# Kernel optimization log

Hardware: AMD Instinct MI355X
Metric: run time of the kernel (lower is better)

Reference implementation:

```python
import jax, jax.numpy as jnp
import numpy as np

N_NODES = 50000
N_RAND_EDGES = 1_600_000
IN_F = 512
HID = 64
HEADS = 8
N_CLASSES = 20
SLOPE = 0.2  # LeakyReLU negative slope


def setup_inputs() -> dict:
    key = jax.random.key(0)
    ks = jax.random.split(key, 6)
    x = jax.random.normal(ks[0], (N_NODES, IN_F), dtype=jnp.float32)
    er = jax.random.randint(ks[1], (2, N_RAND_EDGES), 0, N_NODES)
    loops = jnp.tile(jnp.arange(N_NODES), (2, 1))  # self-loops so every row of adj is nonzero
    edge_index = jnp.concatenate([er, loops], axis=1)  # [2, E]
    # Learned parameters (per SpGraphAttentionLayer: weight [in,out], alpha [1,2*out] -> stored flat)
    W1 = jax.random.normal(ks[2], (HEADS, IN_F, HID), dtype=jnp.float32) * 0.05
    a1 = jax.random.normal(ks[3], (HEADS, 2 * HID), dtype=jnp.float32) * 0.1
    W2 = jax.random.normal(ks[4], (HEADS * HID, N_CLASSES), dtype=jnp.float32) * 0.05
    a2 = jax.random.normal(ks[5], (2 * N_CLASSES,), dtype=jnp.float32) * 0.1
    return {"x": x, "W1": W1, "a1": a1, "W2": W2, "a2": a2, "edge_index": edge_index}


def _gat_layer(x, W, a, e0, e1, n):
    # h = x @ weight; edge score = alpha . [h[src], h[dst]] computed as two per-node dots
    h = x @ W  # [N, F_out]
    f = W.shape[1]
    s_src = h @ a[:f]   # [N]
    s_dst = h @ a[f:]   # [N]
    edge_e = jnp.exp(jax.nn.leaky_relu(s_src[e0] + s_dst[e1], SLOPE))  # [E]
    rowsum = jax.ops.segment_sum(edge_e, e0, num_segments=n)  # spmm(adj_e, ones)
    agg = jax.ops.segment_sum(edge_e[:, None] * h[e1], e0, num_segments=n)  # spmm(adj_e, h)
    return agg / rowsum[:, None]


def reference(x, W1, a1, W2, a2, edge_index):
    n = x.shape[0]
    e0, e1 = edge_index[0], edge_index[1]
    # layer 1: per-head GAT, elu, concat along features (dropout is identity in eval)
    heads = [jax.nn.elu(_gat_layer(x, W1[i], a1[i], e0, e1, n)) for i in range(W1.shape[0])]
    hcat = jnp.concatenate(heads, axis=1)  # [N, HEADS*HID]
    out = jax.nn.elu(_gat_layer(hcat, W2, a2, e0, e1, n))  # [N, C]
    return out
```

## Files before the change

### kernel.cpp

```cpp
#include <hip/hip_runtime.h>
#include <hip/hip_fp16.h>
#include <math.h>

#define SLOPE 0.2f
#define SSHIFT 11

typedef short bf16x8 __attribute__((ext_vector_type(8)));
typedef float f32x4  __attribute__((ext_vector_type(4)));

static __device__ __forceinline__ float elu_f(float x){ return x > 0.f ? x : (__expf(x) - 1.f); }
static __device__ __forceinline__ float lrelu(float t){ return t > 0.f ? t : SLOPE*t; }
static __device__ __forceinline__ unsigned short f2bf_rne(float f){
    unsigned int u = __float_as_uint(f);
    unsigned int r = (u + 0x7FFFu + ((u >> 16) & 1u)) >> 16;
    return (unsigned short)r;
}
static __device__ __forceinline__ float bf2f(unsigned short h){ return __uint_as_float(((unsigned int)h) << 16); }

#define ASYNC_COPY16(gp, lp) \
    __builtin_amdgcn_global_load_lds((const __attribute__((address_space(1))) void*)(gp), \
                                     (__attribute__((address_space(3))) void*)(lp), 16, 0, 0)

__global__ void __launch_bounds__(256) hist_sliced_kernel(const int* __restrict__ e0, const int* __restrict__ e1,
                                                          int E, int n, int NS, int* __restrict__ cnt){
    const int s = blockIdx.x & 7;
    const int c = blockIdx.x >> 3;
    const int K = gridDim.x >> 3;
    const int lo = (int)((long)s*n >> 3), hi = (int)((long)(s+1)*n >> 3);
    const int i0 = (int)((long)c*E/K), i1 = (int)((long)(c+1)*E/K);
    for (int i = i0 + threadIdx.x; i < i1; i += 256){
        int j = e0[i];
        if (j >= lo && j < hi) atomicAdd(&cnt[j*NS + (e1[i] >> SSHIFT)], 1);
    }
}

__global__ void __launch_bounds__(256) scan_reduce_kernel(const int* __restrict__ cnt, int T, int* __restrict__ bsum){
    int c0 = blockIdx.x*4096 + threadIdx.x*16;
    int sum = 0;
    #pragma unroll
    for (int q = 0; q < 16; ++q){ int i = c0 + q; if (i < T) sum += cnt[i]; }
    #pragma unroll
    for (int off = 1; off < 64; off <<= 1) sum += __shfl_xor(sum, off, 64);
    __shared__ int ws_[4];
    int lane = threadIdx.x & 63, wid = threadIdx.x >> 6;
    if (lane == 0) ws_[wid] = sum;
    __syncthreads();
    if (threadIdx.x == 0) bsum[blockIdx.x] = ws_[0] + ws_[1] + ws_[2] + ws_[3];
}

__global__ void __launch_bounds__(512) scan_small_kernel(const int* __restrict__ bsum, int NB, int* __restrict__ bexcl){
    int t = threadIdx.x;
    int v = (t < NB) ? bsum[t] : 0;
    int lane = t & 63, wid = t >> 6;
    int val = v;
    #pragma unroll
    for (int off = 1; off < 64; off <<= 1){ int u = __shfl_up(val, off, 64); if (lane >= off) val += u; }
    __shared__ int wt[8];
    if (lane == 63) wt[wid] = val;
    __syncthreads();
    int base = 0;
    for (int w2 = 0; w2 < wid; ++w2) base += wt[w2];
    if (t < NB) bexcl[t] = base + val - v;
}

__global__ void __launch_bounds__(256) scan_apply_kernel(int* __restrict__ cnt_cur, int T,
                                                         const int* __restrict__ bexcl){
    int c0 = blockIdx.x*4096 + threadIdx.x*16;
    int v[16];
    #pragma unroll
    for (int q = 0; q < 16; ++q){ int i = c0 + q; v[q] = (i < T) ? cnt_cur[i] : 0; }
    int tsum = 0;
    #pragma unroll
    for (int q = 0; q < 16; ++q){ int t_ = v[q]; v[q] = tsum; tsum += t_; }
    int lane = threadIdx.x & 63, wid = threadIdx.x >> 6;
    int val = tsum;
    #pragma unroll
    for (int off = 1; off < 64; off <<= 1){ int u = __shfl_up(val, off, 64); if (lane >= off) val += u; }
    __shared__ int wt[4];
    if (lane == 63) wt[wid] = val;
    __syncthreads();
    int base = bexcl[blockIdx.x];
    for (int w2 = 0; w2 < wid; ++w2) base += wt[w2];
    base += val - tsum;
    #pragma unroll
    for (int q = 0; q < 16; ++q){ int i = c0 + q; if (i < T) cnt_cur[i] = base + v[q]; }
}

__global__ void __launch_bounds__(256) scatter_sliced_kernel(const int* __restrict__ e0, const int* __restrict__ e1,
                                                             int E, int n, int NS,
                                                             int* __restrict__ cursor, int* __restrict__ sidx){
    const int s = blockIdx.x & 7;
    const int c = blockIdx.x >> 3;
    const int K = gridDim.x >> 3;
    const int lo = (int)((long)s*n >> 3), hi = (int)((long)(s+1)*n >> 3);
    const int i0 = (int)((long)c*E/K), i1 = (int)((long)(c+1)*E/K);
    for (int i = i0 + threadIdx.x; i < i1; i += 256){
        int j = e0[i];
        if (j >= lo && j < hi){
            int jj = e1[i];
            int p = atomicAdd(&cursor[j*NS + (jj >> SSHIFT)], 1);
            sidx[p] = jj;
        }
    }
}

__global__ void __launch_bounds__(256) split_x_kernel(const float* __restrict__ x,
                                                      unsigned short* __restrict__ xhi,
                                                      unsigned short* __restrict__ xlo, int total4){
    int i = blockIdx.x*256 + threadIdx.x;
    if (i >= total4) return;
    float4 v = ((const float4*)x)[i];
    ushort4 h, l;
    h.x = f2bf_rne(v.x); l.x = f2bf_rne(v.x - bf2f(h.x));
    h.y = f2bf_rne(v.y); l.y = f2bf_rne(v.y - bf2f(h.y));
    h.z = f2bf_rne(v.z); l.z = f2bf_rne(v.z - bf2f(h.z));
    h.w = f2bf_rne(v.w); l.w = f2bf_rne(v.w - bf2f(h.w));
    ((ushort4*)xhi)[i] = h;
    ((ushort4*)xlo)[i] = l;
}

__global__ void __launch_bounds__(256) prep_w_kernel(const float* __restrict__ W1,
                                                     unsigned short* __restrict__ wThi,
                                                     unsigned short* __restrict__ wTlo){
    int idx = blockIdx.x*256 + threadIdx.x;
    int head = idx >> 15, rem = idx & 32767;
    int c = rem >> 9, k = rem & 511;
    float f = W1[((size_t)head << 15) + k*64 + c];
    unsigned short h = f2bf_rne(f);
    wThi[idx] = h;
    wTlo[idx] = f2bf_rne(f - bf2f(h));
}

__global__ void __launch_bounds__(256) gemm1_mfma_kernel(const unsigned short* __restrict__ xhi,
                                                         const unsigned short* __restrict__ xlo,
                                                         const unsigned short* __restrict__ wThi,
                                                         const unsigned short* __restrict__ wTlo,
                                                         const float* __restrict__ a1,
                                                         __half* __restrict__ h_g,
                                                         float* __restrict__ ssrc, float* __restrict__ sdst,
                                                         int n, int nwg){
    __shared__ unsigned short lds[16384];
    const int bid = blockIdx.x;
    const int xcd = bid & 7, jj = bid >> 3;
    const int q = nwg >> 3, r = nwg & 7;
    const int logical = (xcd < r ? xcd*(q+1) : r*(q+1) + (xcd-r)*q) + jj;
    const int rowtile = logical >> 2, ct = logical & 3;
    const int row0 = rowtile*128, col0 = ct*128;
    const int w = threadIdx.x >> 6, lane = threadIdx.x & 63;
    const int wm = w >> 1, wn = w & 1;
    const int lr = lane & 15, lk = lane >> 4;
    f32x4 acc[4][4] = {};
    const unsigned short* sbase[8];
    unsigned int soff[8];
    #pragma unroll
    for (int i = 0; i < 8; ++i){
        unsigned int off = w*8192u + i*1024u + lane*16u;
        unsigned int arr = off >> 13, within = off & 8191u;
        unsigned int rrow = within >> 6, kel = (within & 63u) >> 1;
        const unsigned short* g;
        size_t gidx;
        if (arr == 0)      { g = xhi;  gidx = (size_t)(row0 + rrow)*512 + kel; }
        else if (arr == 1) { g = xlo;  gidx = (size_t)(row0 + rrow)*512 + kel; }
        else if (arr == 2) { g = wThi; gidx = (size_t)(col0 + rrow)*512 + kel; }
        else               { g = wTlo; gidx = (size_t)(col0 + rrow)*512 + kel; }
        sbase[i] = g + gidx;
        soff[i] = (w*8192u + i*1024u);
    }
    const unsigned short* Ahi = lds;
    const unsigned short* Alo = lds + 4096;
    const unsigned short* Bhi = lds + 8192;
    const unsigned short* Blo = lds + 12288;
    for (int k0 = 0; k0 < 512; k0 += 32){
        #pragma unroll
        for (int i = 0; i < 8; ++i)
            ASYNC_COPY16(sbase[i] + k0, (char*)lds + soff[i]);
        __syncthreads();
        bf16x8 a_h[4], a_l[4], b_h[4], b_l[4];
        #pragma unroll
        for (int mi = 0; mi < 4; ++mi){
            int rowl = wm*64 + mi*16 + lr;
            a_h[mi] = *(const bf16x8*)(Ahi + rowl*32 + lk*8);
            a_l[mi] = *(const bf16x8*)(Alo + rowl*32 + lk*8);
        }
        #pragma unroll
        for (int ni = 0; ni < 4; ++ni){
            int coll = wn*64 + ni*16 + lr;
            b_h[ni] = *(const bf16x8*)(Bhi + coll*32 + lk*8);
            b_l[ni] = *(const bf16x8*)(Blo + coll*32 + lk*8);
        }
        #pragma unroll
        for (int mi = 0; mi < 4; ++mi)
            #pragma unroll
            for (int ni = 0; ni < 4; ++ni){
                f32x4& A = acc[mi][ni];
                A = __builtin_amdgcn_mfma_f32_16x16x32_bf16(a_h[mi], b_h[ni], A, 0, 0, 0);
                A = __builtin_amdgcn_mfma_f32_16x16x32_bf16(a_h[mi], b_l[ni], A, 0, 0, 0);
                A = __builtin_amdgcn_mfma_f32_16x16x32_bf16(a_l[mi], b_h[ni], A, 0, 0, 0);
            }
        __syncthreads();
    }
    const int head = ct*2 + wn;
    float as_[4], ad_[4];
    #pragma unroll
    for (int ni = 0; ni < 4; ++ni){
        as_[ni] = a1[(size_t)head*128 + ni*16 + lr];
        ad_[ni] = a1[(size_t)head*128 + 64 + ni*16 + lr];
    }
    #pragma unroll
    for (int mi = 0; mi < 4; ++mi){
        #pragma unroll
        for (int reg = 0; reg < 4; ++reg){
            float s = 0.f, d = 0.f;
            #pragma unroll
            for (int ni = 0; ni < 4; ++ni){
                float v = acc[mi][ni][reg];
                s += v*as_[ni]; d += v*ad_[ni];
            }
            s += __shfl_xor(s, 1); d += __shfl_xor(d, 1);
            s += __shfl_xor(s, 2); d += __shfl_xor(d, 2);
            s += __shfl_xor(s, 4); d += __shfl_xor(d, 4);
            s += __shfl_xor(s, 8); d += __shfl_xor(d, 8);
            const int node = row0 + wm*64 + mi*16 + lk*4 + reg;
            if (node < n){
                #pragma unroll
                for (int ni = 0; ni < 4; ++ni)
                    h_g[(size_t)node*512 + head*64 + ni*16 + lr] = __float2half(acc[mi][ni][reg]);
                if (lr == 0){
                    ssrc[(size_t)node*8 + head] = s;
                    sdst[(size_t)node*8 + head] = d;
                }
            }
        }
    }
}

__global__ void __launch_bounds__(256) agg1_kernel(const __half* __restrict__ h_g, const float* __restrict__ ssrc,
                                                   const float* __restrict__ sdst,
                                                   const int* __restrict__ bend, const int* __restrict__ sidx,
                                                   __half* __restrict__ hcat, int n, int NS){
    const int w = threadIdx.x >> 6, lane = threadIdx.x & 63;
    const int node = blockIdx.x*4 + w;
    if (node >= n) return;
    const int r0 = node ? bend[(size_t)node*NS - 1] : 0;
    const int r1 = bend[(size_t)(node+1)*NS - 1];
    const int h = lane >> 3;
    const float ssh = ssrc[(size_t)node*8 + h];
    float acc[8] = {};
    float wsum = 0.f;
    int e = r0;
    for (; e + 3 < r1; e += 4){
        int j0 = sidx[e], j1 = sidx[e+1], j2 = sidx[e+2], j3 = sidx[e+3];
        uint4 g0 = *(const uint4*)(h_g + (size_t)j0*512 + lane*8);
        uint4 g1 = *(const uint4*)(h_g + (size_t)j1*512 + lane*8);
        uint4 g2 = *(const uint4*)(h_g + (size_t)j2*512 + lane*8);
        uint4 g3 = *(const uint4*)(h_g + (size_t)j3*512 + lane*8);
        float s0 = sdst[(size_t)j0*8 + h], s1 = sdst[(size_t)j1*8 + h];
        float s2 = sdst[(size_t)j2*8 + h], s3 = sdst[(size_t)j3*8 + h];
        float w0 = __expf(lrelu(ssh + s0));
        float w1 = __expf(lrelu(ssh + s1));
        float w2 = __expf(lrelu(ssh + s2));
        float w3 = __expf(lrelu(ssh + s3));
        const unsigned int* u0 = &g0.x; const unsigned int* u1 = &g1.x;
        const unsigned int* u2 = &g2.x; const unsigned int* u3 = &g3.x;
        #pragma unroll
        for (int qq = 0; qq < 4; ++qq){
            float2 f0 = __half22float2(*(const __half2*)&u0[qq]);
            float2 f1 = __half22float2(*(const __half2*)&u1[qq]);
            float2 f2 = __half22float2(*(const __half2*)&u2[qq]);
            float2 f3 = __half22float2(*(const __half2*)&u3[qq]);
            acc[2*qq]   += w0*f0.x + w1*f1.x + w2*f2.x + w3*f3.x;
            acc[2*qq+1] += w0*f0.y + w1*f1.y + w2*f2.y + w3*f3.y;
        }
        wsum += (w0 + w1) + (w2 + w3);
    }
    for (; e < r1; ++e){
        int j = sidx[e];
        uint4 g = *(const uint4*)(h_g + (size_t)j*512 + lane*8);
        float wg = __expf(lrelu(ssh + sdst[(size_t)j*8 + h]));
        const unsigned int* u = &g.x;
        #pragma unroll
        for (int qq = 0; qq < 4; ++qq){
            float2 f = __half22float2(*(const __half2*)&u[qq]);
            acc[2*qq]   += wg*f.x;
            acc[2*qq+1] += wg*f.y;
        }
        wsum += wg;
    }
    float inv = 1.f / wsum;
    union { uint4 u; __half hv[8]; } pk;
    #pragma unroll
    for (int qq = 0; qq < 8; ++qq) pk.hv[qq] = __float2half(elu_f(acc[qq]*inv));
    *(uint4*)(hcat + (size_t)node*512 + lane*8) = pk.u;
}

__global__ void __launch_bounds__(256) gemm2_kernel(const __half* __restrict__ hcat, const float* __restrict__ W2,
                                                    const float* __restrict__ a2,
                                                    float* __restrict__ h2, float* __restrict__ ssrc,
                                                    float* __restrict__ sdst, int n){
    __shared__ float As[16][257];
    __shared__ float Ws[16][20];
    const int tid = threadIdx.x;
    const int node = blockIdx.x*256 + tid;
    float acc[20] = {};
    for (int k0 = 0; k0 < 512; k0 += 16){
        uint4 u0 = {0,0,0,0}, u1 = {0,0,0,0};
        if (node < n){
            const __half* src = hcat + (size_t)node*512 + k0;
            u0 = *(const uint4*)src;
            u1 = *(const uint4*)(src + 8);
        }
        const unsigned int* ua = &u0.x;
        const unsigned int* ub = &u1.x;
        #pragma unroll
        for (int qq = 0; qq < 4; ++qq){
            float2 f = __half22float2(*(const __half2*)&ua[qq]);
            As[2*qq][tid] = f.x; As[2*qq+1][tid] = f.y;
            float2 g = __half22float2(*(const __half2*)&ub[qq]);
            As[8+2*qq][tid] = g.x; As[8+2*qq+1][tid] = g.y;
        }
        for (int qq = tid; qq < 320; qq += 256){
            int kr = qq/20, cc = qq%20;
            Ws[kr][cc] = W2[(size_t)(k0 + kr)*20 + cc];
        }
        __syncthreads();
        #pragma unroll
        for (int kk = 0; kk < 16; ++kk){
            float a = As[kk][tid];
            #pragma unroll
            for (int cc = 0; cc < 20; ++cc) acc[cc] += a*Ws[kk][cc];
        }
        __syncthreads();
    }
    if (node < n){
        float s0 = 0.f, s1 = 0.f;
        #pragma unroll
        for (int cc = 0; cc < 20; ++cc){
            h2[(size_t)node*20 + cc] = acc[cc];
            s0 += acc[cc]*a2[cc];
            s1 += acc[cc]*a2[20 + cc];
        }
        ssrc[node] = s0; sdst[node] = s1;
    }
}

__global__ void __launch_bounds__(256) agg2_kernel(const float* __restrict__ h2, const float* __restrict__ ssrc,
                                                   const float* __restrict__ sdstv,
                                                   const int* __restrict__ bend, const int* __restrict__ sidx,
                                                   float* __restrict__ out, int n, int NS){
    const int w = threadIdx.x >> 6, lane = threadIdx.x & 63;
    const int node = blockIdx.x*4 + w;
    if (node >= n) return;
    const int r0 = node ? bend[(size_t)node*NS - 1] : 0;
    const int r1 = bend[(size_t)(node+1)*NS - 1];
    const float ss = ssrc[node];
    const bool act = lane < 20;
    float acc = 0.f, wsum = 0.f;
    int e = r0;
    for (; e + 3 < r1; e += 4){
        int j0 = sidx[e], j1 = sidx[e+1], j2 = sidx[e+2], j3 = sidx[e+3];
        float v0 = act ? h2[(size_t)j0*20 + lane] : 0.f;
        float v1 = act ? h2[(size_t)j1*20 + lane] : 0.f;
        float v2 = act ? h2[(size_t)j2*20 + lane] : 0.f;
        float v3 = act ? h2[(size_t)j3*20 + lane] : 0.f;
        float s0 = sdstv[j0], s1 = sdstv[j1], s2 = sdstv[j2], s3 = sdstv[j3];
        float w0 = __expf(lrelu(ss + s0));
        float w1 = __expf(lrelu(ss + s1));
        float w2 = __expf(lrelu(ss + s2));
        float w3 = __expf(lrelu(ss + s3));
        acc += w0*v0 + w1*v1 + w2*v2 + w3*v3;
        wsum += (w0 + w1) + (w2 + w3);
    }
    for (; e < r1; ++e){
        int j = sidx[e];
        float v = act ? h2[(size_t)j*20 + lane] : 0.f;
        float wg = __expf(lrelu(ss + sdstv[j]));
        acc += wg*v; wsum += wg;
    }
    if (act) out[(size_t)node*20 + lane] = elu_f(acc / wsum);
}

extern "C" void kernel_launch(void* const* d_in, const int* in_sizes, int n_in,
                              void* d_out, int out_size, void* d_ws, size_t ws_size,
                              hipStream_t stream){
    const float* x  = (const float*)d_in[0];
    const float* W1 = (const float*)d_in[1];
    const float* a1 = (const float*)d_in[2];
    const float* W2 = (const float*)d_in[3];
    const float* a2 = (const float*)d_in[4];
    const int*   ei = (const int*)d_in[5];
    const int n = in_sizes[0] / 512;
    const int E = in_sizes[5] / 2;
    const int* e0 = ei;
    const int* e1 = ei + E;
    const int NS = (n + (1 << SSHIFT) - 1) >> SSHIFT;
    const int T  = n * NS;

    char* p = (char*)d_ws;
    auto alloc = [&](size_t bytes)->char*{ char* r = p; p += (bytes + 255) & ~(size_t)255; return r; };
    unsigned short* xhi  = (unsigned short*)alloc((size_t)n*512*2);
    unsigned short* xlo  = (unsigned short*)alloc((size_t)n*512*2);
    __half*         h_g  = (__half*)        alloc((size_t)n*512*2);
    unsigned short* wThi = (unsigned short*)alloc((size_t)8*64*512*2);
    unsigned short* wTlo = (unsigned short*)alloc((size_t)8*64*512*2);
    float* ssrc1   = (float*)alloc((size_t)n*8*4);
    float* sdst1   = (float*)alloc((size_t)n*8*4);
    __half* hcat  = (__half*)xhi;
    float*  h2    = (float*)xlo;
    float*  ssrc2 = h2 + (size_t)n*20;
    float*  sdst2 = ssrc2 + n;
    int*    cursor = (int*)((char*)xlo + ((size_t)6 << 20));
    int*    sidx   = cursor + T;
    int*    bsum   = sidx + E;
    int*    bexcl  = bsum + 2048;

    const int total4 = n*512/4;
    split_x_kernel<<<(total4 + 255)/256, 256, 0, stream>>>(x, xhi, xlo, total4);
    prep_w_kernel <<<1024, 256, 0, stream>>>(W1, wThi, wTlo);
    const int mb = (n + 127)/128;
    const int nwg = mb*4;
    gemm1_mfma_kernel<<<nwg, 256, 0, stream>>>(xhi, xlo, wThi, wTlo, a1, h_g, ssrc1, sdst1, n, nwg);

    hipMemsetAsync(cursor, 0, (size_t)T*4, stream);
    const int KCH = 192;
    hist_sliced_kernel<<<KCH*8, 256, 0, stream>>>(e0, e1, E, n, NS, cursor);
    const int NB = (T + 4095)/4096;
    scan_reduce_kernel<<<NB, 256, 0, stream>>>(cursor, T, bsum);
    scan_small_kernel <<<1, 512, 0, stream>>>(bsum, NB, bexcl);
    scan_apply_kernel <<<NB, 256, 0, stream>>>(cursor, T, bexcl);
    scatter_sliced_kernel<<<KCH*8, 256, 0, stream>>>(e0, e1, E, n, NS, cursor, sidx);

    agg1_kernel<<<(n + 3)/4, 256, 0, stream>>>(h_g, ssrc1, sdst1, cursor, sidx, hcat, n, NS);
    const int nb256 = (n + 255)/256;
    gemm2_kernel<<<nb256, 256, 0, stream>>>(hcat, W2, a2, h2, ssrc2, sdst2, n);
    agg2_kernel <<<(n + 3)/4, 256, 0, stream>>>(h2, ssrc2, sdst2, cursor, sidx, (float*)d_out, n, NS);
}
```

Baseline: 835.3 us.

## Precompute per-edge attention weights in scatter, drop column sub-buckets in CSR build

The CSR build no longer sub-buckets each row by destination column slice. Histogram, scan and scatter now work on one counter per node, which shrinks the scan and memset. The scatter kernel now also computes the 8 per-head exp(leakyrelu) edge weights and stores them as bf16 in a per-edge array, so agg1 reads them instead of gathering sdst and computing exp per edge. Both aggregation kernels unroll to 8 edges. In exchange, the per-edge weights lose precision, the weight array adds E*16 bytes of write and read traffic, and the column-sorted locality inside each row that the sub-buckets gave is gone.

```diff
diff --git a/kernel.cpp b/kernel.cpp
--- a/kernel.cpp
+++ b/kernel.cpp
@@ -3,7 +3,6 @@
 #include <math.h>
 
 #define SLOPE 0.2f
-#define SSHIFT 11
 
 typedef short bf16x8 __attribute__((ext_vector_type(8)));
 typedef float f32x4  __attribute__((ext_vector_type(4)));
@@ -21,8 +20,8 @@
     __builtin_amdgcn_global_load_lds((const __attribute__((address_space(1))) void*)(gp), \
                                      (__attribute__((address_space(3))) void*)(lp), 16, 0, 0)
 
-__global__ void __launch_bounds__(256) hist_sliced_kernel(const int* __restrict__ e0, const int* __restrict__ e1,
-                                                          int E, int n, int NS, int* __restrict__ cnt){
+__global__ void __launch_bounds__(256) hist_sliced_kernel(const int* __restrict__ e0, int E, int n,
+                                                          int* __restrict__ cnt){
     const int s = blockIdx.x & 7;
     const int c = blockIdx.x >> 3;
     const int K = gridDim.x >> 3;
@@ -30,7 +29,7 @@
     const int i0 = (int)((long)c*E/K), i1 = (int)((long)(c+1)*E/K);
     for (int i = i0 + threadIdx.x; i < i1; i += 256){
         int j = e0[i];
-        if (j >= lo && j < hi) atomicAdd(&cnt[j*NS + (e1[i] >> SSHIFT)], 1);
+        if (j >= lo && j < hi) atomicAdd(&cnt[j], 1);
     }
 }
 
@@ -86,9 +85,11 @@
     for (int q = 0; q < 16; ++q){ int i = c0 + q; if (i < T) cnt_cur[i] = base + v[q]; }
 }
 
-__global__ void __launch_bounds__(256) scatter_sliced_kernel(const int* __restrict__ e0, const int* __restrict__ e1,
-                                                             int E, int n, int NS,
-                                                             int* __restrict__ cursor, int* __restrict__ sidx){
+__global__ void __launch_bounds__(256) scatter_w_kernel(const int* __restrict__ e0, const int* __restrict__ e1,
+                                                        int E, int n,
+                                                        const float* __restrict__ ssrc1, const float* __restrict__ sdst1,
+                                                        int* __restrict__ cursor, int* __restrict__ sidx,
+                                                        uint4* __restrict__ wgt8){
     const int s = blockIdx.x & 7;
     const int c = blockIdx.x >> 3;
     const int K = gridDim.x >> 3;
@@ -98,8 +99,27 @@
         int j = e0[i];
         if (j >= lo && j < hi){
             int jj = e1[i];
-            int p = atomicAdd(&cursor[j*NS + (jj >> SSHIFT)], 1);
+            int p = atomicAdd(&cursor[j], 1);
             sidx[p] = jj;
+            float4 sa0 = *(const float4*)(ssrc1 + (size_t)j*8);
+            float4 sa1 = *(const float4*)(ssrc1 + (size_t)j*8 + 4);
+            float4 sb0 = *(const float4*)(sdst1 + (size_t)jj*8);
+            float4 sb1 = *(const float4*)(sdst1 + (size_t)jj*8 + 4);
+            float w_[8];
+            w_[0] = __expf(lrelu(sa0.x + sb0.x));
+            w_[1] = __expf(lrelu(sa0.y + sb0.y));
+            w_[2] = __expf(lrelu(sa0.z + sb0.z));
+            w_[3] = __expf(lrelu(sa0.w + sb0.w));
+            w_[4] = __expf(lrelu(sa1.x + sb1.x));
+            w_[5] = __expf(lrelu(sa1.y + sb1.y));
+            w_[6] = __expf(lrelu(sa1.z + sb1.z));
+            w_[7] = __expf(lrelu(sa1.w + sb1.w));
+            uint4 pk;
+            pk.x = (unsigned)f2bf_rne(w_[0]) | ((unsigned)f2bf_rne(w_[1]) << 16);
+            pk.y = (unsigned)f2bf_rne(w_[2]) | ((unsigned)f2bf_rne(w_[3]) << 16);
+            pk.z = (unsigned)f2bf_rne(w_[4]) | ((unsigned)f2bf_rne(w_[5]) << 16);
+            pk.w = (unsigned)f2bf_rne(w_[6]) | ((unsigned)f2bf_rne(w_[7]) << 16);
+            wgt8[p] = pk;
         }
     }
 }
@@ -234,57 +254,54 @@
     }
 }
 
-__global__ void __launch_bounds__(256) agg1_kernel(const __half* __restrict__ h_g, const float* __restrict__ ssrc,
-                                                   const float* __restrict__ sdst,
+__global__ void __launch_bounds__(256) agg1_kernel(const __half* __restrict__ h_g,
+                                                   const unsigned short* __restrict__ wgt,
                                                    const int* __restrict__ bend, const int* __restrict__ sidx,
-                                                   __half* __restrict__ hcat, int n, int NS){
+                                                   __half* __restrict__ hcat, int n){
     const int w = threadIdx.x >> 6, lane = threadIdx.x & 63;
     const int node = blockIdx.x*4 + w;
     if (node >= n) return;
-    const int r0 = node ? bend[(size_t)node*NS - 1] : 0;
-    const int r1 = bend[(size_t)(node+1)*NS - 1];
+    const int r0 = node ? bend[node-1] : 0;
+    const int r1 = bend[node];
     const int h = lane >> 3;
-    const float ssh = ssrc[(size_t)node*8 + h];
     float acc[8] = {};
     float wsum = 0.f;
     int e = r0;
-    for (; e + 3 < r1; e += 4){
-        int j0 = sidx[e], j1 = sidx[e+1], j2 = sidx[e+2], j3 = sidx[e+3];
-        uint4 g0 = *(const uint4*)(h_g + (size_t)j0*512 + lane*8);
-        uint4 g1 = *(const uint4*)(h_g + (size_t)j1*512 + lane*8);
-        uint4 g2 = *(const uint4*)(h_g + (size_t)j2*512 + lane*8);
-        uint4 g3 = *(const uint4*)(h_g + (size_t)j3*512 + lane*8);
-        float s0 = sdst[(size_t)j0*8 + h], s1 = sdst[(size_t)j1*8 + h];
-        float s2 = sdst[(size_t)j2*8 + h], s3 = sdst[(size_t)j3*8 + h];
-        float w0 = __expf(lrelu(ssh + s0));
-        float w1 = __expf(lrelu(ssh + s1));
-        float w2 = __expf(lrelu(ssh + s2));
-        float w3 = __expf(lrelu(ssh + s3));
-        const unsigned int* u0 = &g0.x; const unsigned int* u1 = &g1.x;
-        const unsigned int* u2 = &g2.x; const unsigned int* u3 = &g3.x;
-        #pragma unroll
-        for (int qq = 0; qq < 4; ++qq){
-            float2 f0 = __half22float2(*(const __half2*)&u0[qq]);
-            float2 f1 = __half22float2(*(const __half2*)&u1[qq]);
-            float2 f2 = __half22float2(*(const __half2*)&u2[qq]);
-            float2 f3 = __half22float2(*(const __half2*)&u3[qq]);
-            acc[2*qq]   += w0*f0.x + w1*f1.x + w2*f2.x + w3*f3.x;
-            acc[2*qq+1] += w0*f0.y + w1*f1.y + w2*f2.y + w3*f3.y;
-        }
-        wsum += (w0 + w1) + (w2 + w3);
+    for (; e + 7 < r1; e += 8){
+        int j[8];
+        #pragma unroll
+        for (int qq = 0; qq < 8; ++qq) j[qq] = sidx[e+qq];
+        uint4 g[8];
+        #pragma unroll
+        for (int qq = 0; qq < 8; ++qq) g[qq] = *(const uint4*)(h_g + (size_t)j[qq]*512 + lane*8);
+        float wv[8];
+        #pragma unroll
+        for (int qq = 0; qq < 8; ++qq) wv[qq] = bf2f(wgt[(size_t)(e+qq)*8 + h]);
+        #pragma unroll
+        for (int qq = 0; qq < 8; ++qq){
+            const unsigned int* u = &g[qq].x;
+            float wq = wv[qq];
+            #pragma unroll
+            for (int p2 = 0; p2 < 4; ++p2){
+                float2 f = __half22float2(*(const __half2*)&u[p2]);
+                acc[2*p2]   += wq*f.x;
+                acc[2*p2+1] += wq*f.y;
+            }
+            wsum += wq;
+        }
     }
     for (; e < r1; ++e){
         int j = sidx[e];
         uint4 g = *(const uint4*)(h_g + (size_t)j*512 + lane*8);
-        float wg = __expf(lrelu(ssh + sdst[(size_t)j*8 + h]));
+        float wq = bf2f(wgt[(size_t)e*8 + h]);
         const unsigned int* u = &g.x;
         #pragma unroll
-        for (int qq = 0; qq < 4; ++qq){
-            float2 f = __half22float2(*(const __half2*)&u[qq]);
-            acc[2*qq]   += wg*f.x;
-            acc[2*qq+1] += wg*f.y;
-        }
-        wsum += wg;
+        for (int p2 = 0; p2 < 4; ++p2){
+            float2 f = __half22float2(*(const __half2*)&u[p2]);
+            acc[2*p2]   += wq*f.x;
+            acc[2*p2+1] += wq*f.y;
+        }
+        wsum += wq;
     }
     float inv = 1.f / wsum;
     union { uint4 u; __half hv[8]; } pk;
@@ -346,35 +363,37 @@
 __global__ void __launch_bounds__(256) agg2_kernel(const float* __restrict__ h2, const float* __restrict__ ssrc,
                                                    const float* __restrict__ sdstv,
                                                    const int* __restrict__ bend, const int* __restrict__ sidx,
-                                                   float* __restrict__ out, int n, int NS){
+                                                   float* __restrict__ out, int n){
     const int w = threadIdx.x >> 6, lane = threadIdx.x & 63;
     const int node = blockIdx.x*4 + w;
     if (node >= n) return;
-    const int r0 = node ? bend[(size_t)node*NS - 1] : 0;
-    const int r1 = bend[(size_t)(node+1)*NS - 1];
+    const int r0 = node ? bend[node-1] : 0;
+    const int r1 = bend[node];
     const float ss = ssrc[node];
     const bool act = lane < 20;
     float acc = 0.f, wsum = 0.f;
     int e = r0;
-    for (; e + 3 < r1; e += 4){
-        int j0 = sidx[e], j1 = sidx[e+1], j2 = sidx[e+2], j3 = sidx[e+3];
-        float v0 = act ? h2[(size_t)j0*20 + lane] : 0.f;
-        float v1 = act ? h2[(size_t)j1*20 + lane] : 0.f;
-        float v2 = act ? h2[(size_t)j2*20 + lane] : 0.f;
-        float v3 = act ? h2[(size_t)j3*20 + lane] : 0.f;
-        float s0 = sdstv[j0], s1 = sdstv[j1], s2 = sdstv[j2], s3 = sdstv[j3];
-        float w0 = __expf(lrelu(ss + s0));
-        float w1 = __expf(lrelu(ss + s1));
-        float w2 = __expf(lrelu(ss + s2));
-        float w3 = __expf(lrelu(ss + s3));
-        acc += w0*v0 + w1*v1 + w2*v2 + w3*v3;
-        wsum += (w0 + w1) + (w2 + w3);
+    for (; e + 7 < r1; e += 8){
+        int j[8];
+        #pragma unroll
+        for (int qq = 0; qq < 8; ++qq) j[qq] = sidx[e+qq];
+        float v[8], s[8];
+        #pragma unroll
+        for (int qq = 0; qq < 8; ++qq) v[qq] = act ? h2[(size_t)j[qq]*20 + lane] : 0.f;
+        #pragma unroll
+        for (int qq = 0; qq < 8; ++qq) s[qq] = sdstv[j[qq]];
+        #pragma unroll
+        for (int qq = 0; qq < 8; ++qq){
+            float wq = __expf(lrelu(ss + s[qq]));
+            acc += wq*v[qq];
+            wsum += wq;
+        }
     }
     for (; e < r1; ++e){
         int j = sidx[e];
         float v = act ? h2[(size_t)j*20 + lane] : 0.f;
-        float wg = __expf(lrelu(ss + sdstv[j]));
-        acc += wg*v; wsum += wg;
+        float wq = __expf(lrelu(ss + sdstv[j]));
+        acc += wq*v; wsum += wq;
     }
     if (act) out[(size_t)node*20 + lane] = elu_f(acc / wsum);
 }
@@ -392,8 +411,6 @@
     const int E = in_sizes[5] / 2;
     const int* e0 = ei;
     const int* e1 = ei + E;
-    const int NS = (n + (1 << SSHIFT) - 1) >> SSHIFT;
-    const int T  = n * NS;
 
     char* p = (char*)d_ws;
     auto alloc = [&](size_t bytes)->char*{ char* r = p; p += (bytes + 255) & ~(size_t)255; return r; };
@@ -405,13 +422,16 @@
     float* ssrc1   = (float*)alloc((size_t)n*8*4);
     float* sdst1   = (float*)alloc((size_t)n*8*4);
     __half* hcat  = (__half*)xhi;
-    float*  h2    = (float*)xlo;
-    float*  ssrc2 = h2 + (size_t)n*20;
-    float*  sdst2 = ssrc2 + n;
-    int*    cursor = (int*)((char*)xlo + ((size_t)6 << 20));
-    int*    sidx   = cursor + T;
-    int*    bsum   = sidx + E;
-    int*    bexcl  = bsum + 2048;
+    char* q2 = (char*)xlo;
+    auto alloc2 = [&](size_t bytes)->char*{ char* r = q2; q2 += (bytes + 255) & ~(size_t)255; return r; };
+    float* h2    = (float*)alloc2((size_t)n*20*4);
+    float* ssrc2 = (float*)alloc2((size_t)n*4);
+    float* sdst2 = (float*)alloc2((size_t)n*4);
+    int*   cursor = (int*)  alloc2((size_t)n*4);
+    int*   sidx   = (int*)  alloc2((size_t)E*4);
+    int*   bsum   = (int*)  alloc2(4096);
+    int*   bexcl  = (int*)  alloc2(4096);
+    uint4* wgt8   = (uint4*)alloc2((size_t)E*16);
 
     const int total4 = n*512/4;
     split_x_kernel<<<(total4 + 255)/256, 256, 0, stream>>>(x, xhi, xlo, total4);
@@ -420,17 +440,17 @@
     const int nwg = mb*4;
     gemm1_mfma_kernel<<<nwg, 256, 0, stream>>>(xhi, xlo, wThi, wTlo, a1, h_g, ssrc1, sdst1, n, nwg);
 
-    hipMemsetAsync(cursor, 0, (size_t)T*4, stream);
+    hipMemsetAsync(cursor, 0, (size_t)n*4, stream);
     const int KCH = 192;
-    hist_sliced_kernel<<<KCH*8, 256, 0, stream>>>(e0, e1, E, n, NS, cursor);
-    const int NB = (T + 4095)/4096;
-    scan_reduce_kernel<<<NB, 256, 0, stream>>>(cursor, T, bsum);
+    hist_sliced_kernel<<<KCH*8, 256, 0, stream>>>(e0, E, n, cursor);
+    const int NB = (n + 4095)/4096;
+    scan_reduce_kernel<<<NB, 256, 0, stream>>>(cursor, n, bsum);
     scan_small_kernel <<<1, 512, 0, stream>>>(bsum, NB, bexcl);
-    scan_apply_kernel <<<NB, 256, 0, stream>>>(cursor, T, bexcl);
-    scatter_sliced_kernel<<<KCH*8, 256, 0, stream>>>(e0, e1, E, n, NS, cursor, sidx);
-
-    agg1_kernel<<<(n + 3)/4, 256, 0, stream>>>(h_g, ssrc1, sdst1, cursor, sidx, hcat, n, NS);
+    scan_apply_kernel <<<NB, 256, 0, stream>>>(cursor, n, bexcl);
+    scatter_w_kernel  <<<KCH*8, 256, 0, stream>>>(e0, e1, E, n, ssrc1, sdst1, cursor, sidx, wgt8);
+
+    agg1_kernel<<<(n + 3)/4, 256, 0, stream>>>(h_g, (const unsigned short*)wgt8, cursor, sidx, hcat, n);
     const int nb256 = (n + 255)/256;
     gemm2_kernel<<<nb256, 256, 0, stream>>>(hcat, W2, a2, h2, ssrc2, sdst2, n);
-    agg2_kernel <<<(n + 3)/4, 256, 0, stream>>>(h2, ssrc2, sdst2, cursor, sidx, (float*)d_out, n, NS);
-}
+    agg2_kernel <<<(n + 3)/4, 256, 0, stream>>>(h2, ssrc2, sdst2, cursor, sidx, (float*)d_out, n);
+}
```

Measured after the change: 867.6 us. +3.9%, slower.
